# Kernel tuning notes

Measured on AMD Instinct MI355X. Metric: run time of the kernel, lower is better.

Reference implementation:

```python
import jax, jax.numpy as jnp
import numpy as np

N = 200_000      # active voxels
C_IN = 128
C_OUT = 128
GRID = 128
K = 27           # 3x3x3 submanifold kernel offsets
EPS = 1e-4       # scn BatchNormalization default eps
LEAK = 0.333     # scn LeakyReLU default leakiness


def _build_neighbor_idx(rng):
    # unique active voxel coords via unique linear keys in GRID^3
    keys = rng.choice(GRID ** 3, size=N, replace=False).astype(np.int64)
    z = keys % GRID
    y = (keys // GRID) % GRID
    x = keys // (GRID * GRID)
    coords = np.stack([x, y, z], axis=1)  # [N,3]
    order = np.argsort(keys)
    sorted_keys = keys[order]
    offs = np.array([(dx, dy, dz) for dx in (-1, 0, 1)
                     for dy in (-1, 0, 1) for dz in (-1, 0, 1)], dtype=np.int64)
    nb = np.full((N, K), -1, dtype=np.int32)
    for k in range(K):
        q = coords + offs[k]  # [N,3]
        inb = np.all((q >= 0) & (q < GRID), axis=1)
        qk = (q[:, 0] * GRID + q[:, 1]) * GRID + q[:, 2]
        pos = np.searchsorted(sorted_keys, qk)
        pos = np.clip(pos, 0, N - 1)
        hit = inb & (sorted_keys[pos] == qk)
        nb[:, k] = np.where(hit, order[pos].astype(np.int32), -1)
    return nb


def setup_inputs() -> dict:
    key = jax.random.key(0)
    k1, k2 = jax.random.split(key)
    rng = np.random.default_rng(0)
    neighbor_idx = jnp.asarray(_build_neighbor_idx(rng))       # [N,27] int32, -1 = inactive
    features = jax.random.normal(k1, (N, C_IN), dtype=jnp.float32)
    # per-offset conv weights, scn-style init scale
    W = jax.random.normal(k2, (K, C_IN, C_OUT), dtype=jnp.float32) * (1.0 / np.sqrt(K * C_IN))
    b = jnp.zeros((C_OUT,), dtype=jnp.float32)
    gamma = jnp.ones((C_OUT,), dtype=jnp.float32)
    beta = jnp.zeros((C_OUT,), dtype=jnp.float32)
    return {"features": features, "W": W, "b": b, "gamma": gamma,
            "beta": beta, "neighbor_idx": neighbor_idx}


def reference(features, W, b, gamma, beta, neighbor_idx):
    # Submanifold 3D conv: output only at active sites; gather active neighbors.
    valid = (neighbor_idx >= 0)                      # [N,27] bool
    idx = jnp.where(valid, neighbor_idx, 0)          # safe gather index
    out = jnp.broadcast_to(b, (features.shape[0], C_OUT))
    for k in range(K):  # fixed structural loop over 27 kernel offsets
        xk = features[idx[:, k]] * valid[:, k:k + 1].astype(features.dtype)  # [N,C_IN]
        out = out + xk @ W[k]                                                # [N,C_OUT]
    # BatchNormalization over all active sites (training-mode batch stats)
    mean = jnp.mean(out, axis=0)
    var = jnp.var(out, axis=0)
    out = (out - mean) * jax.lax.rsqrt(var + EPS) * gamma + beta
    # LeakyReLU (scn default leakiness 0.333)
    return jnp.where(out > 0, out, LEAK * out)
```

## Files before the change

kernel.cpp:

```cpp
#include <hip/hip_runtime.h>
#include <hip/hip_bf16.h>

#define N_VOX 200000
#define CI 128
#define CO 128
#define KK 27
#define BM 128
#define NBLK 1563
#define NSTEP 54
#define LEAK 0.333f
#define BN_EPS 1e-4f

typedef unsigned short u16;
typedef unsigned int u32;
typedef __attribute__((ext_vector_type(8))) short short8;
typedef __attribute__((ext_vector_type(4))) float f32x4;

typedef const __attribute__((address_space(1))) u32* gptr_t;
typedef __attribute__((address_space(3))) u32* lptr_t;

__device__ __forceinline__ u16 f2bf(float f) {
  union { float f; u32 u; } x; x.f = f;
  return (u16)((x.u + 0x7FFFu + ((x.u >> 16) & 1u)) >> 16);
}
__device__ __forceinline__ u16 cvt_bf(float f) {
  union { __hip_bfloat16 h; u16 u; } c;
  c.h = __float2bfloat16(f);
  return c.u;
}

__global__ __launch_bounds__(256) void fcast_kernel(const float* __restrict__ f,
                                                    u16* __restrict__ fb) {
  size_t i = ((size_t)blockIdx.x * 256 + threadIdx.x) * 8;
  float4 a = *(const float4*)(f + i);
  float4 b = *(const float4*)(f + i + 4);
  u16 t[8];
  t[0] = cvt_bf(a.x); t[1] = cvt_bf(a.y); t[2] = cvt_bf(a.z); t[3] = cvt_bf(a.w);
  t[4] = cvt_bf(b.x); t[5] = cvt_bf(b.y); t[6] = cvt_bf(b.z); t[7] = cvt_bf(b.w);
  *(uint4*)(fb + i) = *(const uint4*)t;
}

__global__ __launch_bounds__(256) void wcast2_kernel(const float* __restrict__ W,
                                                     u16* __restrict__ Wt2) {
  int gid = blockIdx.x * 256 + threadIdx.x;
  int lane = gid & 63, chunk = gid >> 6;
  int n8 = chunk & 7, ks = (chunk >> 3) & 1, half = (chunk >> 4) & 1, k = chunk >> 5;
  int lr = lane & 15, lg = lane >> 4;
  int co = n8 * 16 + lr;
  int ci0 = half * 64 + ks * 32 + lg * 8;
  const float* Wk = W + (size_t)k * CI * CO;
  u16 t[8];
#pragma unroll
  for (int e = 0; e < 8; ++e) t[e] = f2bf(Wk[(ci0 + e) * CO + co]);
  *(uint4*)(Wt2 + (size_t)gid * 8) = *(const uint4*)t;
}

__global__ __launch_bounds__(256, 2) void conv_kernel(
    const u16* __restrict__ featb, const u16* __restrict__ Wt2,
    const int* __restrict__ nb, const u16* __restrict__ zp,
    float* __restrict__ out, float* __restrict__ partial) {
  __shared__ __align__(16) char smem[79360];
  int* const nbs = (int*)(smem + 65536);
  float* const sq = (float*)smem;

  const int tid = threadIdx.x;
  const int bid = blockIdx.x;
  const int row0 = bid * BM;

  for (int i = tid; i < BM * KK; i += 256) {
    int gi = row0 * KK + i;
    nbs[i] = (gi < N_VOX * KK) ? nb[gi] : -1;
  }
  __syncthreads();

  const int lane = tid & 63;
  const int wv = tid >> 6;
  const int wr = wv >> 1, wc = wv & 1;
  const int lr = lane & 15, lg = lane >> 4;

  f32x4 acc[4][4];
#pragma unroll
  for (int m = 0; m < 4; ++m)
#pragma unroll
    for (int n = 0; n < 4; ++n) acc[m][n] = (f32x4){0.f, 0.f, 0.f, 0.f};

  short8 b0[8], b1[8];

  auto issueA = [&](int s, int slot) {
    if (s >= NSTEP) s = NSTEP - 1;
    int k = s >> 1;
    int halfU = (s & 1) * 64;
    u16* Adst = (u16*)(smem + slot * 16384);
    int r = tid >> 3, cl = tid & 7;
#pragma unroll
    for (int j = 0; j < 4; ++j) {
      int row = j * 32 + r;
      int src = nbs[row * KK + k];
      const u16* g = (src >= 0) ? (featb + (size_t)src * CI + halfU) : zp;
      g += ((cl ^ (row & 7)) << 3);
      __builtin_amdgcn_global_load_lds((gptr_t)g, (lptr_t)(Adst + (j * 32 + wv * 8) * 64),
                                       16, 0, 0);
    }
  };

  auto loadB = [&](int s, short8* bn) {
    if (s >= NSTEP) s = NSTEP - 1;
    int k = s >> 1, half = s & 1;
    const u16* base = Wt2 + (((k * 2 + half) * 16 + wc * 4) * 512) + lane * 8;
#pragma unroll
    for (int n = 0; n < 4; ++n)
#pragma unroll
      for (int ks = 0; ks < 2; ++ks)
        bn[n * 2 + ks] = *(const short8*)(base + (ks * 8 + n) * 512);
  };

  auto compute = [&](int slot, const short8* bc) {
    const char* A = smem + slot * 16384;
    __builtin_amdgcn_s_setprio(1);
#pragma unroll
    for (int ks = 0; ks < 2; ++ks) {
      short8 a[4];
#pragma unroll
      for (int m = 0; m < 4; ++m) {
        int r = wr * 64 + m * 16 + lr;
        a[m] = *(const short8*)(A + r * 128 + ((ks * 64 + lg * 16) ^ ((r & 7) << 4)));
      }
#pragma unroll
      for (int m = 0; m < 4; ++m)
#pragma unroll
        for (int n = 0; n < 4; ++n)
          acc[m][n] = __builtin_amdgcn_mfma_f32_16x16x32_bf16(a[m], bc[n * 2 + ks],
                                                              acc[m][n], 0, 0, 0);
    }
    __builtin_amdgcn_s_setprio(0);
  };

  auto step_body = [&](int s, const short8* bc, short8* bn) {
    asm volatile("s_waitcnt vmcnt(16)" ::: "memory");
    __builtin_amdgcn_sched_barrier(0);
    __builtin_amdgcn_s_barrier();
    __builtin_amdgcn_sched_barrier(0);
    loadB(s + 1, bn);
    issueA(s + 3, (s + 3) & 3);
    compute(s & 3, bc);
  };

  issueA(0, 0);
  issueA(1, 1);
  loadB(0, b0);
  issueA(2, 2);
  for (int s = 0; s < NSTEP; s += 2) {
    step_body(s, b0, b1);
    step_body(s + 1, b1, b0);
  }

  float sv[4], qv[4];
#pragma unroll
  for (int n = 0; n < 4; ++n) {
    float s = 0.f, q = 0.f;
    int col = wc * 64 + n * 16 + lr;
#pragma unroll
    for (int m = 0; m < 4; ++m) {
      int rb = row0 + wr * 64 + m * 16 + lg * 4;
#pragma unroll
      for (int e = 0; e < 4; ++e) {
        float x = acc[m][n][e];
        if (rb + e < N_VOX) out[(size_t)(rb + e) * CO + col] = x;
        s += x; q += x * x;
      }
    }
    s += __shfl_xor(s, 16, 64); s += __shfl_xor(s, 32, 64);
    q += __shfl_xor(q, 16, 64); q += __shfl_xor(q, 32, 64);
    sv[n] = s; qv[n] = q;
  }
  __syncthreads();
  if (lg == 0) {
#pragma unroll
    for (int n = 0; n < 4; ++n) {
      int col = wc * 64 + n * 16 + lr;
      sq[wr * 256 + col] = sv[n];
      sq[wr * 256 + 128 + col] = qv[n];
    }
  }
  __syncthreads();
  partial[(size_t)bid * 256 + tid] = sq[tid] + sq[256 + tid];
}

__global__ __launch_bounds__(256, 2) void conv_fb_kernel(
    const float* __restrict__ feat, const u16* __restrict__ Wt2,
    const int* __restrict__ nb, float* __restrict__ out,
    float* __restrict__ partial) {
  __shared__ __align__(16) char smem[46592];
  u16* const Ab = (u16*)smem;
  int* const nbs = (int*)(smem + 32768);
  float* const sq = (float*)smem;

  const int tid = threadIdx.x;
  const int bid = blockIdx.x;
  const int row0 = bid * BM;

  for (int i = tid; i < BM * KK; i += 256) {
    int gi = row0 * KK + i;
    nbs[i] = (gi < N_VOX * KK) ? nb[gi] : -1;
  }
  __syncthreads();

  const int lane = tid & 63;
  const int wv = tid >> 6;
  const int wr = wv >> 1, wc = wv & 1;
  const int lr = lane & 15, lg = lane >> 4;
  const int arow = tid >> 1;
  const int acol = (tid & 1) * 32;

  f32x4 acc[4][4];
#pragma unroll
  for (int m = 0; m < 4; ++m)
#pragma unroll
    for (int n = 0; n < 4; ++n) acc[m][n] = (f32x4){0.f, 0.f, 0.f, 0.f};

  float4 af[8];
  short8 b0[8], b1[8];

  auto issueAf = [&](int s) {
    int k = s >> 1, half = (s & 1) * 64;
    int src = nbs[arow * KK + k];
    if (src >= 0) {
      const float4* p = (const float4*)(feat + (size_t)src * CI + half + acol);
#pragma unroll
      for (int j = 0; j < 8; ++j) af[j] = p[j];
    } else {
#pragma unroll
      for (int j = 0; j < 8; ++j) af[j] = (float4){0.f, 0.f, 0.f, 0.f};
    }
  };
  auto loadB = [&](int s, short8* bn) {
    int k = s >> 1, half = s & 1;
    const u16* base = Wt2 + (((k * 2 + half) * 16 + wc * 4) * 512) + lane * 8;
#pragma unroll
    for (int n = 0; n < 4; ++n)
#pragma unroll
      for (int ks = 0; ks < 2; ++ks)
        bn[n * 2 + ks] = *(const short8*)(base + (ks * 8 + n) * 512);
  };
  auto writeA = [&](u16* Adst) {
    int v = arow & 7;
#pragma unroll
    for (int q = 0; q < 4; ++q) {
      u16 t8[8];
#pragma unroll
      for (int i = 0; i < 2; ++i) {
        float4 f = af[q * 2 + i];
        t8[i * 4 + 0] = cvt_bf(f.x); t8[i * 4 + 1] = cvt_bf(f.y);
        t8[i * 4 + 2] = cvt_bf(f.z); t8[i * 4 + 3] = cvt_bf(f.w);
      }
      int c_o = (tid & 1) * 4 + q;
      *(uint4*)&Adst[arow * 64 + ((c_o ^ v) << 3)] = *(const uint4*)t8;
    }
  };
  auto compute = [&](const u16* A, const short8* bc) {
#pragma unroll
    for (int ks = 0; ks < 2; ++ks) {
      short8 a[4];
#pragma unroll
      for (int m = 0; m < 4; ++m) {
        int r = wr * 64 + m * 16 + lr;
        a[m] = *(const short8*)((const char*)A + r * 128 +
                                ((ks * 64 + lg * 16) ^ ((r & 7) << 4)));
      }
#pragma unroll
      for (int m = 0; m < 4; ++m)
#pragma unroll
        for (int n = 0; n < 4; ++n)
          acc[m][n] = __builtin_amdgcn_mfma_f32_16x16x32_bf16(a[m], bc[n * 2 + ks],
                                                              acc[m][n], 0, 0, 0);
    }
  };

  issueAf(0);
  loadB(0, b0);
  for (int s = 0; s + 2 <= NSTEP - 1; s += 2) {
    writeA(Ab + (s & 1) * 8192); __syncthreads();
    issueAf(s + 1); loadB(s + 1, b1);
    compute(Ab + (s & 1) * 8192, b0);
    writeA(Ab + ((s + 1) & 1) * 8192); __syncthreads();
    issueAf(s + 2); loadB(s + 2, b0);
    compute(Ab + ((s + 1) & 1) * 8192, b1);
  }
  writeA(Ab); __syncthreads();
  issueAf(NSTEP - 1); loadB(NSTEP - 1, b1);
  compute(Ab, b0);
  writeA(Ab + 8192); __syncthreads();
  compute(Ab + 8192, b1);

  float sv[4], qv[4];
#pragma unroll
  for (int n = 0; n < 4; ++n) {
    float s = 0.f, q = 0.f;
    int col = wc * 64 + n * 16 + lr;
#pragma unroll
    for (int m = 0; m < 4; ++m) {
      int rb = row0 + wr * 64 + m * 16 + lg * 4;
#pragma unroll
      for (int e = 0; e < 4; ++e) {
        float x = acc[m][n][e];
        if (rb + e < N_VOX) out[(size_t)(rb + e) * CO + col] = x;
        s += x; q += x * x;
      }
    }
    s += __shfl_xor(s, 16, 64); s += __shfl_xor(s, 32, 64);
    q += __shfl_xor(q, 16, 64); q += __shfl_xor(q, 32, 64);
    sv[n] = s; qv[n] = q;
  }
  __syncthreads();
  if (lg == 0) {
#pragma unroll
    for (int n = 0; n < 4; ++n) {
      int col = wc * 64 + n * 16 + lr;
      sq[wr * 256 + col] = sv[n];
      sq[wr * 256 + 128 + col] = qv[n];
    }
  }
  __syncthreads();
  partial[(size_t)bid * 256 + tid] = sq[tid] + sq[256 + tid];
}

__global__ __launch_bounds__(256) void reduce1_kernel(const float* __restrict__ partial,
                                                      float* __restrict__ partial2) {
  int t = threadIdx.x, b = blockIdx.x;
  float acc = 0.f;
  int jend = (b + 1) * 16; if (jend > NBLK) jend = NBLK;
  for (int j = b * 16; j < jend; ++j) acc += partial[(size_t)j * 256 + t];
  partial2[(size_t)b * 256 + t] = acc;
}

__global__ __launch_bounds__(256) void reduce2_kernel(const float* __restrict__ partial2,
                                                      const float* __restrict__ gamma,
                                                      const float* __restrict__ beta,
                                                      float* __restrict__ stats) {
  __shared__ float sums[256];
  int t = threadIdx.x;
  float acc = 0.f;
  for (int j = 0; j < 98; ++j) acc += partial2[(size_t)j * 256 + t];
  sums[t] = acc;
  __syncthreads();
  if (t < 128) {
    float mean = sums[t] / (float)N_VOX;
    float var = sums[128 + t] / (float)N_VOX - mean * mean;
    float scale = gamma[t] * rsqrtf(var + BN_EPS);
    stats[t] = scale;
    stats[128 + t] = beta[t] - mean * scale;
  }
}

__global__ __launch_bounds__(256) void bnact_kernel(float* __restrict__ out,
                                                    const float* __restrict__ stats) {
  __shared__ float s_scale[128], s_shift[128];
  int t = threadIdx.x;
  if (t < 128) { s_scale[t] = stats[t]; s_shift[t] = stats[128 + t]; }
  __syncthreads();
  size_t i = (size_t)blockIdx.x * 256 + t;
  float4* o4 = (float4*)out;
  float4 v = o4[i];
  int c0 = ((int)(i & 31)) << 2;
  float x;
  x = v.x * s_scale[c0 + 0] + s_shift[c0 + 0]; v.x = x > 0.f ? x : LEAK * x;
  x = v.y * s_scale[c0 + 1] + s_shift[c0 + 1]; v.y = x > 0.f ? x : LEAK * x;
  x = v.z * s_scale[c0 + 2] + s_shift[c0 + 2]; v.z = x > 0.f ? x : LEAK * x;
  x = v.w * s_scale[c0 + 3] + s_shift[c0 + 3]; v.w = x > 0.f ? x : LEAK * x;
  o4[i] = v;
}

extern "C" void kernel_launch(void* const* d_in, const int* in_sizes, int n_in,
                              void* d_out, int out_size, void* d_ws, size_t ws_size,
                              hipStream_t stream) {
  const float* feat  = (const float*)d_in[0];
  const float* W     = (const float*)d_in[1];
  const float* gamma = (const float*)d_in[3];
  const float* beta  = (const float*)d_in[4];
  const int*   nb    = (const int*)d_in[5];
  float* out = (float*)d_out;

  char* ws = (char*)d_ws;
  u16*   Wt2      = (u16*)ws;
  float* partial  = (float*)(ws + 884736);
  float* partial2 = (float*)(ws + 2485248);
  float* stats    = (float*)(ws + 2585600);
  u16*   zp       = (u16*)(ws + 2586624);
  u16*   featb    = (u16*)(ws + 2586880);
  const size_t need_fast = 2586880u + 51200000u;

  hipLaunchKernelGGL(wcast2_kernel, dim3(216), dim3(256), 0, stream, W, Wt2);
  if (ws_size >= need_fast) {
    hipMemsetAsync(zp, 0, 256, stream);
    hipLaunchKernelGGL(fcast_kernel, dim3(12500), dim3(256), 0, stream, feat, featb);
    hipLaunchKernelGGL(conv_kernel, dim3(NBLK), dim3(256), 0, stream,
                       featb, Wt2, nb, zp, out, partial);
  } else {
    hipLaunchKernelGGL(conv_fb_kernel, dim3(NBLK), dim3(256), 0, stream,
                       feat, Wt2, nb, out, partial);
  }
  hipLaunchKernelGGL(reduce1_kernel, dim3(98), dim3(256), 0, stream, partial, partial2);
  hipLaunchKernelGGL(reduce2_kernel, dim3(1), dim3(256), 0, stream, partial2, gamma, beta, stats);
  hipLaunchKernelGGL(bnact_kernel, dim3(25000), dim3(256), 0, stream, out, stats);
}
```

Measured before the change: 303.7 us.

## Compact valid neighbors per offset and skip inactive rows in sparse conv

The dense conv kernel, which gathered all 128 rows for every one of the 27 offsets, is replaced by a sparse variant. Per block it uses ballots to compact the valid (row, source) pairs for each offset into LDS lists padded to multiples of 16. It then runs MFMA only over those compacted tiles and scatter-accumulates the results into an LDS fp32 accumulator, with the centre offset handled first as a plain store. Weights are re-laid out so each wave keeps its own 32-column slice in registers per offset. The aim is to cut MFMA and gather work in proportion to neighbor sparsity. In exchange it drops the async LDS pipelining and caps each offset list at 64 entries, which would silently drop neighbors in denser inputs.

Measured after the change: 294.5 us. 3.0% less time.

```diff
diff --git a/kernel.cpp b/kernel.cpp
--- a/kernel.cpp
+++ b/kernel.cpp
@@ -10,6 +10,8 @@
 #define NSTEP 54
 #define LEAK 0.333f
 #define BN_EPS 1e-4f
+#define SENT 0x3FFFFu
+#define ACC_STRIDE 132
 
 typedef unsigned short u16;
 typedef unsigned int u32;
@@ -40,154 +42,151 @@
   *(uint4*)(fb + i) = *(const uint4*)t;
 }
 
-__global__ __launch_bounds__(256) void wcast2_kernel(const float* __restrict__ W,
-                                                     u16* __restrict__ Wt2) {
+__global__ __launch_bounds__(256) void wcast3_kernel(const float* __restrict__ W,
+                                                     u16* __restrict__ Wt3) {
   int gid = blockIdx.x * 256 + threadIdx.x;
   int lane = gid & 63, chunk = gid >> 6;
-  int n8 = chunk & 7, ks = (chunk >> 3) & 1, half = (chunk >> 4) & 1, k = chunk >> 5;
+  int ks = chunk & 3, nf = (chunk >> 2) & 7, k = chunk >> 5;
   int lr = lane & 15, lg = lane >> 4;
-  int co = n8 * 16 + lr;
-  int ci0 = half * 64 + ks * 32 + lg * 8;
+  int co = nf * 16 + lr;
+  int ci0 = ks * 32 + lg * 8;
   const float* Wk = W + (size_t)k * CI * CO;
   u16 t[8];
 #pragma unroll
   for (int e = 0; e < 8; ++e) t[e] = f2bf(Wk[(ci0 + e) * CO + co]);
-  *(uint4*)(Wt2 + (size_t)gid * 8) = *(const uint4*)t;
-}
-
-__global__ __launch_bounds__(256, 2) void conv_kernel(
-    const u16* __restrict__ featb, const u16* __restrict__ Wt2,
+  *(uint4*)(Wt3 + (size_t)gid * 8) = *(const uint4*)t;
+}
+
+__global__ __launch_bounds__(256, 2) void conv_sp_kernel(
+    const u16* __restrict__ featb, const u16* __restrict__ Wt3,
     const int* __restrict__ nb, const u16* __restrict__ zp,
     float* __restrict__ out, float* __restrict__ partial) {
-  __shared__ __align__(16) char smem[79360];
-  int* const nbs = (int*)(smem + 65536);
-  float* const sq = (float*)smem;
+  __shared__ __align__(16) char smem[75776];
+  float* const accf = (float*)smem;
+  u32* const rb_lds = (u32*)(smem + 67584);
+  int* const cnt_lds = (int*)(smem + 74752);
+  int* const wcnt = (int*)(smem + 74864);
+  float* const ps = (float*)(smem + 67584);
 
   const int tid = threadIdx.x;
   const int bid = blockIdx.x;
   const int row0 = bid * BM;
-
-  for (int i = tid; i < BM * KK; i += 256) {
-    int gi = row0 * KK + i;
-    nbs[i] = (gi < N_VOX * KK) ? nb[gi] : -1;
-  }
-  __syncthreads();
-
   const int lane = tid & 63;
-  const int wv = tid >> 6;
-  const int wr = wv >> 1, wc = wv & 1;
+  const int w = tid >> 6;
+
+  {
+    const bool inrow = (tid < 128) && (row0 + tid < N_VOX);
+    const int* nbp = nb + (size_t)(row0 + tid) * KK;
+    int vv[KK];
+#pragma unroll
+    for (int k = 0; k < KK; ++k) vv[k] = (k != 13 && inrow) ? nbp[k] : -1;
+    if (tid < 128)
+      rb_lds[832 + tid] = ((u32)tid << 18) | (inrow ? (u32)(row0 + tid) : SENT);
+    if (tid == 0) cnt_lds[13] = 128;
+#pragma unroll
+    for (int k = 0; k < KK; ++k) {
+      if (k == 13) continue;
+      bool valid = vv[k] >= 0;
+      unsigned long long m = __ballot(valid);
+      if (lane == 0) wcnt[w] = (int)__popcll(m);
+      __syncthreads();
+      int pos = (int)__popcll(m & ((1ull << lane) - 1ull)) + (w == 1 ? wcnt[0] : 0);
+      int cnt = wcnt[0] + wcnt[1]; if (cnt > 64) cnt = 64;
+      int kbase = (k < 13) ? k * 64 : 960 + (k - 14) * 64;
+      if (valid && pos < 64) rb_lds[kbase + pos] = ((u32)tid << 18) | (u32)vv[k];
+      int pe = (cnt + 15) & ~15;
+      for (int i = cnt + tid; i < pe; i += 256) rb_lds[kbase + i] = SENT;
+      if (tid == 0) cnt_lds[k] = cnt;
+      __syncthreads();
+    }
+  }
+
+  const int wv = w;
   const int lr = lane & 15, lg = lane >> 4;
-
-  f32x4 acc[4][4];
-#pragma unroll
-  for (int m = 0; m < 4; ++m)
-#pragma unroll
-    for (int n = 0; n < 4; ++n) acc[m][n] = (f32x4){0.f, 0.f, 0.f, 0.f};
-
-  short8 b0[8], b1[8];
-
-  auto issueA = [&](int s, int slot) {
-    if (s >= NSTEP) s = NSTEP - 1;
-    int k = s >> 1;
-    int halfU = (s & 1) * 64;
-    u16* Adst = (u16*)(smem + slot * 16384);
-    int r = tid >> 3, cl = tid & 7;
-#pragma unroll
-    for (int j = 0; j < 4; ++j) {
-      int row = j * 32 + r;
-      int src = nbs[row * KK + k];
-      const u16* g = (src >= 0) ? (featb + (size_t)src * CI + halfU) : zp;
-      g += ((cl ^ (row & 7)) << 3);
-      __builtin_amdgcn_global_load_lds((gptr_t)g, (lptr_t)(Adst + (j * 32 + wv * 8) * 64),
-                                       16, 0, 0);
-    }
-  };
-
-  auto loadB = [&](int s, short8* bn) {
-    if (s >= NSTEP) s = NSTEP - 1;
-    int k = s >> 1, half = s & 1;
-    const u16* base = Wt2 + (((k * 2 + half) * 16 + wc * 4) * 512) + lane * 8;
-#pragma unroll
-    for (int n = 0; n < 4; ++n)
-#pragma unroll
-      for (int ks = 0; ks < 2; ++ks)
-        bn[n * 2 + ks] = *(const short8*)(base + (ks * 8 + n) * 512);
-  };
-
-  auto compute = [&](int slot, const short8* bc) {
-    const char* A = smem + slot * 16384;
-    __builtin_amdgcn_s_setprio(1);
-#pragma unroll
-    for (int ks = 0; ks < 2; ++ks) {
+  const int colbase = wv * 32 + lr;
+
+  for (int kk = 0; kk < KK; ++kk) {
+    const int k = (kk == 0) ? 13 : (kk <= 13 ? kk - 1 : kk);
+    const int kbase = (k < 13) ? k * 64 : (k == 13 ? 832 : 960 + (k - 14) * 64);
+    const int cnt = cnt_lds[k];
+    if (cnt == 0) continue;
+    const int nt = (cnt + 15) >> 4;
+    short8 b0[4], b1[4];
+    {
+      const u16* wb = Wt3 + (size_t)(k * 32 + wv * 8) * 512 + lane * 8;
+#pragma unroll
+      for (int ks = 0; ks < 4; ++ks) {
+        b0[ks] = *(const short8*)(wb + ks * 512);
+        b1[ks] = *(const short8*)(wb + (4 + ks) * 512);
+      }
+    }
+    for (int t = 0; t < nt; ++t) {
+      u32 es = rb_lds[kbase + t * 16 + lr];
+      u32 src = es & SENT;
+      const u16* ap = (src == SENT) ? zp : (featb + (size_t)src * CI);
       short8 a[4];
 #pragma unroll
-      for (int m = 0; m < 4; ++m) {
-        int r = wr * 64 + m * 16 + lr;
-        a[m] = *(const short8*)(A + r * 128 + ((ks * 64 + lg * 16) ^ ((r & 7) << 4)));
-      }
-#pragma unroll
-      for (int m = 0; m < 4; ++m)
-#pragma unroll
-        for (int n = 0; n < 4; ++n)
-          acc[m][n] = __builtin_amdgcn_mfma_f32_16x16x32_bf16(a[m], bc[n * 2 + ks],
-                                                              acc[m][n], 0, 0, 0);
-    }
-    __builtin_amdgcn_s_setprio(0);
-  };
-
-  auto step_body = [&](int s, const short8* bc, short8* bn) {
-    asm volatile("s_waitcnt vmcnt(16)" ::: "memory");
-    __builtin_amdgcn_sched_barrier(0);
-    __builtin_amdgcn_s_barrier();
-    __builtin_amdgcn_sched_barrier(0);
-    loadB(s + 1, bn);
-    issueA(s + 3, (s + 3) & 3);
-    compute(s & 3, bc);
-  };
-
-  issueA(0, 0);
-  issueA(1, 1);
-  loadB(0, b0);
-  issueA(2, 2);
-  for (int s = 0; s < NSTEP; s += 2) {
-    step_body(s, b0, b1);
-    step_body(s + 1, b1, b0);
-  }
-
-  float sv[4], qv[4];
-#pragma unroll
-  for (int n = 0; n < 4; ++n) {
-    float s = 0.f, q = 0.f;
-    int col = wc * 64 + n * 16 + lr;
-#pragma unroll
-    for (int m = 0; m < 4; ++m) {
-      int rb = row0 + wr * 64 + m * 16 + lg * 4;
-#pragma unroll
-      for (int e = 0; e < 4; ++e) {
-        float x = acc[m][n][e];
-        if (rb + e < N_VOX) out[(size_t)(rb + e) * CO + col] = x;
-        s += x; q += x * x;
-      }
-    }
-    s += __shfl_xor(s, 16, 64); s += __shfl_xor(s, 32, 64);
-    q += __shfl_xor(q, 16, 64); q += __shfl_xor(q, 32, 64);
-    sv[n] = s; qv[n] = q;
-  }
-  __syncthreads();
-  if (lg == 0) {
-#pragma unroll
-    for (int n = 0; n < 4; ++n) {
-      int col = wc * 64 + n * 16 + lr;
-      sq[wr * 256 + col] = sv[n];
-      sq[wr * 256 + 128 + col] = qv[n];
-    }
-  }
-  __syncthreads();
-  partial[(size_t)bid * 256 + tid] = sq[tid] + sq[256 + tid];
+      for (int ks = 0; ks < 4; ++ks) a[ks] = *(const short8*)(ap + ks * 32 + lg * 8);
+      f32x4 c0 = {0.f, 0.f, 0.f, 0.f}, c1 = {0.f, 0.f, 0.f, 0.f};
+#pragma unroll
+      for (int ks = 0; ks < 4; ++ks) {
+        c0 = __builtin_amdgcn_mfma_f32_16x16x32_bf16(a[ks], b0[ks], c0, 0, 0, 0);
+        c1 = __builtin_amdgcn_mfma_f32_16x16x32_bf16(a[ks], b1[ks], c1, 0, 0, 0);
+      }
+      if (kk == 0) {
+#pragma unroll
+        for (int r = 0; r < 4; ++r) {
+          int dr = (int)(rb_lds[kbase + t * 16 + lg * 4 + r] >> 18);
+          accf[dr * ACC_STRIDE + colbase] = c0[r];
+          accf[dr * ACC_STRIDE + colbase + 16] = c1[r];
+        }
+      } else {
+#pragma unroll
+        for (int r = 0; r < 4; ++r) {
+          u32 e2 = rb_lds[kbase + t * 16 + lg * 4 + r];
+          if (e2 != SENT) {
+            int dr = (int)(e2 >> 18);
+            accf[dr * ACC_STRIDE + colbase] += c0[r];
+            accf[dr * ACC_STRIDE + colbase + 16] += c1[r];
+          }
+        }
+      }
+    }
+  }
+  __syncthreads();
+
+  float s4[4] = {0.f, 0.f, 0.f, 0.f}, q4[4] = {0.f, 0.f, 0.f, 0.f};
+  const int col4 = (tid & 31) * 4;
+  const int rgrp = tid >> 5;
+#pragma unroll
+  for (int i = 0; i < 16; ++i) {
+    int row = rgrp + i * 8;
+    f32x4 v = *(const f32x4*)&accf[row * ACC_STRIDE + col4];
+    int grow = row0 + row;
+    if (grow < N_VOX) {
+      *(float4*)&out[(size_t)grow * CO + col4] = *(float4*)&v;
+#pragma unroll
+      for (int j = 0; j < 4; ++j) { s4[j] += v[j]; q4[j] += v[j] * v[j]; }
+    }
+  }
+  __syncthreads();
+#pragma unroll
+  for (int j = 0; j < 4; ++j) {
+    ps[rgrp * 128 + col4 + j] = s4[j];
+    ps[1024 + rgrp * 128 + col4 + j] = q4[j];
+  }
+  __syncthreads();
+  {
+    int col = tid & 127, which = tid >> 7;
+    float acc = 0.f;
+#pragma unroll
+    for (int g = 0; g < 8; ++g) acc += ps[which * 1024 + g * 128 + col];
+    partial[(size_t)bid * 256 + tid] = acc;
+  }
 }
 
 __global__ __launch_bounds__(256, 2) void conv_fb_kernel(
-    const float* __restrict__ feat, const u16* __restrict__ Wt2,
+    const float* __restrict__ feat, const u16* __restrict__ Wt3,
     const int* __restrict__ nb, float* __restrict__ out,
     float* __restrict__ partial) {
   __shared__ __align__(16) char smem[46592];
@@ -235,12 +234,12 @@
   };
   auto loadB = [&](int s, short8* bn) {
     int k = s >> 1, half = s & 1;
-    const u16* base = Wt2 + (((k * 2 + half) * 16 + wc * 4) * 512) + lane * 8;
 #pragma unroll
     for (int n = 0; n < 4; ++n)
 #pragma unroll
       for (int ks = 0; ks < 2; ++ks)
-        bn[n * 2 + ks] = *(const short8*)(base + (ks * 8 + n) * 512);
+        bn[n * 2 + ks] = *(const short8*)(Wt3 +
+            (size_t)((k * 32 + (wc * 4 + n) * 4) + half * 2 + ks) * 512 + lane * 8);
   };
   auto writeA = [&](u16* Adst) {
     int v = arow & 7;
@@ -299,11 +298,11 @@
     int col = wc * 64 + n * 16 + lr;
 #pragma unroll
     for (int m = 0; m < 4; ++m) {
-      int rb = row0 + wr * 64 + m * 16 + lg * 4;
+      int rb_ = row0 + wr * 64 + m * 16 + lg * 4;
 #pragma unroll
       for (int e = 0; e < 4; ++e) {
         float x = acc[m][n][e];
-        if (rb + e < N_VOX) out[(size_t)(rb + e) * CO + col] = x;
+        if (rb_ + e < N_VOX) out[(size_t)(rb_ + e) * CO + col] = x;
         s += x; q += x * x;
       }
     }
@@ -381,23 +380,23 @@
   float* out = (float*)d_out;
 
   char* ws = (char*)d_ws;
-  u16*   Wt2      = (u16*)ws;
+  u16*   Wt3      = (u16*)ws;
   float* partial  = (float*)(ws + 884736);
   float* partial2 = (float*)(ws + 2485248);
   float* stats    = (float*)(ws + 2585600);
   u16*   zp       = (u16*)(ws + 2586624);
   u16*   featb    = (u16*)(ws + 2586880);
-  const size_t need_fast = 2586880u + 51200000u;
-
-  hipLaunchKernelGGL(wcast2_kernel, dim3(216), dim3(256), 0, stream, W, Wt2);
+  const size_t need_fast = 53786880u;
+
+  hipLaunchKernelGGL(wcast3_kernel, dim3(216), dim3(256), 0, stream, W, Wt3);
   if (ws_size >= need_fast) {
     hipMemsetAsync(zp, 0, 256, stream);
     hipLaunchKernelGGL(fcast_kernel, dim3(12500), dim3(256), 0, stream, feat, featb);
-    hipLaunchKernelGGL(conv_kernel, dim3(NBLK), dim3(256), 0, stream,
-                       featb, Wt2, nb, zp, out, partial);
+    hipLaunchKernelGGL(conv_sp_kernel, dim3(NBLK), dim3(256), 0, stream,
+                       featb, Wt3, nb, zp, out, partial);
   } else {
     hipLaunchKernelGGL(conv_fb_kernel, dim3(NBLK), dim3(256), 0, stream,
-                       feat, Wt2, nb, out, partial);
+                       feat, Wt3, nb, out, partial);
   }
   hipLaunchKernelGGL(reduce1_kernel, dim3(98), dim3(256), 0, stream, partial, partial2);
   hipLaunchKernelGGL(reduce2_kernel, dim3(1), dim3(256), 0, stream, partial2, gamma, beta, stats);
```

## Stage weights through LDS with 512-thread blocks and triple-buffered A/B pipeline

Applied to the files above, without the earlier changes.

The main conv kernel now uses 512-thread blocks with 8 waves, each wave computing a 32x64 sub-tile. Weight tiles are staged into LDS with global_load_lds alongside the gathered feature rows, in a 3-slot ring buffer, instead of being loaded into registers per wave. A new transposed, XOR-swizzled weight cast kernel supports this layout, and block IDs are remapped so each XCD gets a contiguous range of rows, which should improve L2 locality of neighbor gathers. The change cuts register pressure and duplicated B loads across waves. In exchange it adds an extra barrier per half-step and uses far more LDS per block, which may limit occupancy.

Result: slower. 360.0 us (+18.5%).

```diff
diff --git a/kernel.cpp b/kernel.cpp
--- a/kernel.cpp
+++ b/kernel.cpp
@@ -40,119 +40,137 @@
   *(uint4*)(fb + i) = *(const uint4*)t;
 }
 
-__global__ __launch_bounds__(256) void wcast2_kernel(const float* __restrict__ W,
-                                                     u16* __restrict__ Wt2) {
+__global__ __launch_bounds__(256) void wcast_kernel(const float* __restrict__ W,
+                                                    u16* __restrict__ Wt) {
+  __shared__ float tile[32][33];
+  int k = blockIdx.z;
+  int ci0 = blockIdx.y * 32, co0 = blockIdx.x * 32;
+  const float* Wk = W + (size_t)k * CI * CO;
+  u16* Wtk = Wt + (size_t)k * CI * CO;
+  int tx = threadIdx.x, ty = threadIdx.y;
+#pragma unroll
+  for (int j = 0; j < 4; ++j)
+    tile[ty + j * 8][tx] = Wk[(ci0 + ty + j * 8) * CO + co0 + tx];
+  __syncthreads();
+#pragma unroll
+  for (int j = 0; j < 4; ++j) {
+    int co = co0 + ty + j * 8;
+    int ci = ci0 + tx;
+    Wtk[co * CI + (ci ^ ((co & 7) << 3))] = f2bf(tile[tx][ty + j * 8]);
+  }
+}
+
+__global__ __launch_bounds__(256) void wcast3_kernel(const float* __restrict__ W,
+                                                     u16* __restrict__ Wt3) {
   int gid = blockIdx.x * 256 + threadIdx.x;
   int lane = gid & 63, chunk = gid >> 6;
-  int n8 = chunk & 7, ks = (chunk >> 3) & 1, half = (chunk >> 4) & 1, k = chunk >> 5;
+  int ks = chunk & 3, nf = (chunk >> 2) & 7, k = chunk >> 5;
   int lr = lane & 15, lg = lane >> 4;
-  int co = n8 * 16 + lr;
-  int ci0 = half * 64 + ks * 32 + lg * 8;
+  int co = nf * 16 + lr;
+  int ci0 = ks * 32 + lg * 8;
   const float* Wk = W + (size_t)k * CI * CO;
   u16 t[8];
 #pragma unroll
   for (int e = 0; e < 8; ++e) t[e] = f2bf(Wk[(ci0 + e) * CO + co]);
-  *(uint4*)(Wt2 + (size_t)gid * 8) = *(const uint4*)t;
-}
-
-__global__ __launch_bounds__(256, 2) void conv_kernel(
-    const u16* __restrict__ featb, const u16* __restrict__ Wt2,
+  *(uint4*)(Wt3 + (size_t)gid * 8) = *(const uint4*)t;
+}
+
+__global__ __launch_bounds__(512, 2) void conv_dn_kernel(
+    const u16* __restrict__ featb, const u16* __restrict__ Wt,
     const int* __restrict__ nb, const u16* __restrict__ zp,
     float* __restrict__ out, float* __restrict__ partial) {
-  __shared__ __align__(16) char smem[79360];
-  int* const nbs = (int*)(smem + 65536);
-  float* const sq = (float*)smem;
+  __shared__ __align__(16) char smem[112128];
+  int* const nbs = (int*)(smem + 98304);
+  float* const ps = (float*)smem;
 
   const int tid = threadIdx.x;
-  const int bid = blockIdx.x;
+  const int orig = blockIdx.x;
+  const int xcd = orig & 7, oidx = orig >> 3;
+  const int bid = (xcd < 3) ? xcd * 196 + oidx : 588 + (xcd - 3) * 195 + oidx;
   const int row0 = bid * BM;
-
-  for (int i = tid; i < BM * KK; i += 256) {
+  const int lane = tid & 63;
+  const int w = tid >> 6;
+  const int wr = w >> 1, wc = w & 1;
+  const int lr = lane & 15, lg = lane >> 4;
+
+  for (int i = tid; i < BM * KK; i += 512) {
     int gi = row0 * KK + i;
     nbs[i] = (gi < N_VOX * KK) ? nb[gi] : -1;
   }
   __syncthreads();
 
-  const int lane = tid & 63;
-  const int wv = tid >> 6;
-  const int wr = wv >> 1, wc = wv & 1;
-  const int lr = lane & 15, lg = lane >> 4;
-
-  f32x4 acc[4][4];
-#pragma unroll
-  for (int m = 0; m < 4; ++m)
+  f32x4 acc[2][4];
+#pragma unroll
+  for (int m = 0; m < 2; ++m)
 #pragma unroll
     for (int n = 0; n < 4; ++n) acc[m][n] = (f32x4){0.f, 0.f, 0.f, 0.f};
 
-  short8 b0[8], b1[8];
-
-  auto issueA = [&](int s, int slot) {
-    if (s >= NSTEP) s = NSTEP - 1;
-    int k = s >> 1;
-    int halfU = (s & 1) * 64;
-    u16* Adst = (u16*)(smem + slot * 16384);
-    int r = tid >> 3, cl = tid & 7;
-#pragma unroll
-    for (int j = 0; j < 4; ++j) {
-      int row = j * 32 + r;
+  auto stage = [&](int s, int slot) {
+    int k = s >> 1, half = (s & 1) * 64;
+    u16* Aslot = (u16*)(smem + slot * 32768);
+    u16* Bslot = Aslot + 8192;
+#pragma unroll
+    for (int j = 0; j < 2; ++j) {
+      int cid = j * 512 + tid;
+      int row = cid >> 3, c = cid & 7;
       int src = nbs[row * KK + k];
-      const u16* g = (src >= 0) ? (featb + (size_t)src * CI + halfU) : zp;
-      g += ((cl ^ (row & 7)) << 3);
-      __builtin_amdgcn_global_load_lds((gptr_t)g, (lptr_t)(Adst + (j * 32 + wv * 8) * 64),
-                                       16, 0, 0);
-    }
-  };
-
-  auto loadB = [&](int s, short8* bn) {
-    if (s >= NSTEP) s = NSTEP - 1;
-    int k = s >> 1, half = s & 1;
-    const u16* base = Wt2 + (((k * 2 + half) * 16 + wc * 4) * 512) + lane * 8;
-#pragma unroll
-    for (int n = 0; n < 4; ++n)
-#pragma unroll
-      for (int ks = 0; ks < 2; ++ks)
-        bn[n * 2 + ks] = *(const short8*)(base + (ks * 8 + n) * 512);
-  };
-
-  auto compute = [&](int slot, const short8* bc) {
-    const char* A = smem + slot * 16384;
+      const u16* g = (src >= 0) ? (featb + (size_t)src * CI + half) : zp;
+      g += ((c ^ (row & 7)) << 3);
+      __builtin_amdgcn_global_load_lds((gptr_t)g,
+          (lptr_t)(Aslot + (j * 512 + w * 64) * 8), 16, 0, 0);
+    }
+#pragma unroll
+    for (int j = 0; j < 2; ++j) {
+      int cid = j * 512 + tid;
+      int co = cid >> 3, sub = cid & 7;
+      __builtin_amdgcn_global_load_lds(
+          (gptr_t)(Wt + (size_t)k * CI * CO + co * CI + half + sub * 8),
+          (lptr_t)(Bslot + (j * 512 + w * 64) * 8), 16, 0, 0);
+    }
+  };
+
+  auto phase = [&](const u16* A, const u16* B, int ks) {
+    short8 a[2], b[4];
+#pragma unroll
+    for (int m = 0; m < 2; ++m) {
+      int r = wr * 32 + m * 16 + lr;
+      a[m] = *(const short8*)((const char*)(A + r * 64) +
+                              ((ks * 64 + lg * 16) ^ ((r & 7) << 4)));
+    }
+#pragma unroll
+    for (int n = 0; n < 4; ++n) {
+      int cn = wc * 64 + n * 16 + lr;
+      b[n] = *(const short8*)((const char*)(B + cn * 64) +
+                              ((ks * 64 + lg * 16) ^ ((cn & 7) << 4)));
+    }
     __builtin_amdgcn_s_setprio(1);
 #pragma unroll
-    for (int ks = 0; ks < 2; ++ks) {
-      short8 a[4];
-#pragma unroll
-      for (int m = 0; m < 4; ++m) {
-        int r = wr * 64 + m * 16 + lr;
-        a[m] = *(const short8*)(A + r * 128 + ((ks * 64 + lg * 16) ^ ((r & 7) << 4)));
-      }
-#pragma unroll
-      for (int m = 0; m < 4; ++m)
-#pragma unroll
-        for (int n = 0; n < 4; ++n)
-          acc[m][n] = __builtin_amdgcn_mfma_f32_16x16x32_bf16(a[m], bc[n * 2 + ks],
-                                                              acc[m][n], 0, 0, 0);
-    }
+    for (int m = 0; m < 2; ++m)
+#pragma unroll
+      for (int n = 0; n < 4; ++n)
+        acc[m][n] = __builtin_amdgcn_mfma_f32_16x16x32_bf16(a[m], b[n], acc[m][n], 0, 0, 0);
     __builtin_amdgcn_s_setprio(0);
   };
 
-  auto step_body = [&](int s, const short8* bc, short8* bn) {
-    asm volatile("s_waitcnt vmcnt(16)" ::: "memory");
+  stage(0, 0);
+  stage(1, 1);
+  for (int s = 0; s < NSTEP; ++s) {
+    asm volatile("s_waitcnt vmcnt(4)" ::: "memory");
     __builtin_amdgcn_sched_barrier(0);
     __builtin_amdgcn_s_barrier();
     __builtin_amdgcn_sched_barrier(0);
-    loadB(s + 1, bn);
-    issueA(s + 3, (s + 3) & 3);
-    compute(s & 3, bc);
-  };
-
-  issueA(0, 0);
-  issueA(1, 1);
-  loadB(0, b0);
-  issueA(2, 2);
-  for (int s = 0; s < NSTEP; s += 2) {
-    step_body(s, b0, b1);
-    step_body(s + 1, b1, b0);
-  }
+    int sn = (s + 2 < NSTEP) ? s + 2 : NSTEP - 1;
+    stage(sn, (s + 2) % 3);
+    const u16* A = (const u16*)(smem + (s % 3) * 32768);
+    const u16* B = A + 8192;
+    phase(A, B, 0);
+    __builtin_amdgcn_sched_barrier(0);
+    __builtin_amdgcn_s_barrier();
+    __builtin_amdgcn_sched_barrier(0);
+    phase(A, B, 1);
+  }
+  asm volatile("s_waitcnt vmcnt(0)" ::: "memory");
+  __syncthreads();
 
   float sv[4], qv[4];
 #pragma unroll
@@ -160,13 +178,15 @@
     float s = 0.f, q = 0.f;
     int col = wc * 64 + n * 16 + lr;
 #pragma unroll
-    for (int m = 0; m < 4; ++m) {
-      int rb = row0 + wr * 64 + m * 16 + lg * 4;
+    for (int m = 0; m < 2; ++m) {
+      int rb = row0 + wr * 32 + m * 16 + lg * 4;
 #pragma unroll
       for (int e = 0; e < 4; ++e) {
         float x = acc[m][n][e];
-        if (rb + e < N_VOX) out[(size_t)(rb + e) * CO + col] = x;
-        s += x; q += x * x;
+        if (rb + e < N_VOX) {
+          out[(size_t)(rb + e) * CO + col] = x;
+          s += x; q += x * x;
+        }
       }
     }
     s += __shfl_xor(s, 16, 64); s += __shfl_xor(s, 32, 64);
@@ -178,16 +198,21 @@
 #pragma unroll
     for (int n = 0; n < 4; ++n) {
       int col = wc * 64 + n * 16 + lr;
-      sq[wr * 256 + col] = sv[n];
-      sq[wr * 256 + 128 + col] = qv[n];
-    }
-  }
-  __syncthreads();
-  partial[(size_t)bid * 256 + tid] = sq[tid] + sq[256 + tid];
+      ps[wr * 256 + col] = sv[n];
+      ps[wr * 256 + 128 + col] = qv[n];
+    }
+  }
+  __syncthreads();
+  if (tid < 256) {
+    float acc2 = 0.f;
+#pragma unroll
+    for (int g = 0; g < 4; ++g) acc2 += ps[g * 256 + tid];
+    partial[(size_t)bid * 256 + tid] = acc2;
+  }
 }
 
 __global__ __launch_bounds__(256, 2) void conv_fb_kernel(
-    const float* __restrict__ feat, const u16* __restrict__ Wt2,
+    const float* __restrict__ feat, const u16* __restrict__ Wt3,
     const int* __restrict__ nb, float* __restrict__ out,
     float* __restrict__ partial) {
   __shared__ __align__(16) char smem[46592];
@@ -197,9 +222,9 @@
 
   const int tid = threadIdx.x;
   const int bid = blockIdx.x;
-  const int row0 = bid * BM;
-
-  for (int i = tid; i < BM * KK; i += 256) {
+  const int row0 = bid * 128;
+
+  for (int i = tid; i < 128 * KK; i += 256) {
     int gi = row0 * KK + i;
     nbs[i] = (gi < N_VOX * KK) ? nb[gi] : -1;
   }
@@ -235,12 +260,12 @@
   };
   auto loadB = [&](int s, short8* bn) {
     int k = s >> 1, half = s & 1;
-    const u16* base = Wt2 + (((k * 2 + half) * 16 + wc * 4) * 512) + lane * 8;
 #pragma unroll
     for (int n = 0; n < 4; ++n)
 #pragma unroll
       for (int ks = 0; ks < 2; ++ks)
-        bn[n * 2 + ks] = *(const short8*)(base + (ks * 8 + n) * 512);
+        bn[n * 2 + ks] = *(const short8*)(Wt3 +
+            (size_t)((k * 32 + (wc * 4 + n) * 4) + half * 2 + ks) * 512 + lane * 8);
   };
   auto writeA = [&](u16* Adst) {
     int v = arow & 7;
@@ -299,11 +324,11 @@
     int col = wc * 64 + n * 16 + lr;
 #pragma unroll
     for (int m = 0; m < 4; ++m) {
-      int rb = row0 + wr * 64 + m * 16 + lg * 4;
+      int rb_ = row0 + wr * 64 + m * 16 + lg * 4;
 #pragma unroll
       for (int e = 0; e < 4; ++e) {
         float x = acc[m][n][e];
-        if (rb + e < N_VOX) out[(size_t)(rb + e) * CO + col] = x;
+        if (rb_ + e < N_VOX) out[(size_t)(rb_ + e) * CO + col] = x;
         s += x; q += x * x;
       }
     }
@@ -325,10 +350,11 @@
 }
 
 __global__ __launch_bounds__(256) void reduce1_kernel(const float* __restrict__ partial,
-                                                      float* __restrict__ partial2) {
+                                                      float* __restrict__ partial2,
+                                                      int nblk) {
   int t = threadIdx.x, b = blockIdx.x;
   float acc = 0.f;
-  int jend = (b + 1) * 16; if (jend > NBLK) jend = NBLK;
+  int jend = (b + 1) * 16; if (jend > nblk) jend = nblk;
   for (int j = b * 16; j < jend; ++j) acc += partial[(size_t)j * 256 + t];
   partial2[(size_t)b * 256 + t] = acc;
 }
@@ -336,11 +362,11 @@
 __global__ __launch_bounds__(256) void reduce2_kernel(const float* __restrict__ partial2,
                                                       const float* __restrict__ gamma,
                                                       const float* __restrict__ beta,
-                                                      float* __restrict__ stats) {
+                                                      float* __restrict__ stats, int n2) {
   __shared__ float sums[256];
   int t = threadIdx.x;
   float acc = 0.f;
-  for (int j = 0; j < 98; ++j) acc += partial2[(size_t)j * 256 + t];
+  for (int j = 0; j < n2; ++j) acc += partial2[(size_t)j * 256 + t];
   sums[t] = acc;
   __syncthreads();
   if (t < 128) {
@@ -381,25 +407,32 @@
   float* out = (float*)d_out;
 
   char* ws = (char*)d_ws;
-  u16*   Wt2      = (u16*)ws;
+  u16*   Wt       = (u16*)ws;
   float* partial  = (float*)(ws + 884736);
   float* partial2 = (float*)(ws + 2485248);
   float* stats    = (float*)(ws + 2585600);
   u16*   zp       = (u16*)(ws + 2586624);
   u16*   featb    = (u16*)(ws + 2586880);
-  const size_t need_fast = 2586880u + 51200000u;
-
-  hipLaunchKernelGGL(wcast2_kernel, dim3(216), dim3(256), 0, stream, W, Wt2);
+  const size_t need_fast = 53786880u;
+
   if (ws_size >= need_fast) {
+    hipLaunchKernelGGL(wcast_kernel, dim3(4, 4, 27), dim3(32, 8), 0, stream, W, Wt);
     hipMemsetAsync(zp, 0, 256, stream);
     hipLaunchKernelGGL(fcast_kernel, dim3(12500), dim3(256), 0, stream, feat, featb);
-    hipLaunchKernelGGL(conv_kernel, dim3(NBLK), dim3(256), 0, stream,
-                       featb, Wt2, nb, zp, out, partial);
+    hipLaunchKernelGGL(conv_dn_kernel, dim3(NBLK), dim3(512), 0, stream,
+                       featb, Wt, nb, zp, out, partial);
+    hipLaunchKernelGGL(reduce1_kernel, dim3(98), dim3(256), 0, stream,
+                       partial, partial2, NBLK);
+    hipLaunchKernelGGL(reduce2_kernel, dim3(1), dim3(256), 0, stream,
+                       partial2, gamma, beta, stats, 98);
   } else {
+    hipLaunchKernelGGL(wcast3_kernel, dim3(216), dim3(256), 0, stream, W, Wt);
     hipLaunchKernelGGL(conv_fb_kernel, dim3(NBLK), dim3(256), 0, stream,
-                       feat, Wt2, nb, out, partial);
-  }
-  hipLaunchKernelGGL(reduce1_kernel, dim3(98), dim3(256), 0, stream, partial, partial2);
-  hipLaunchKernelGGL(reduce2_kernel, dim3(1), dim3(256), 0, stream, partial2, gamma, beta, stats);
+                       feat, Wt, nb, out, partial);
+    hipLaunchKernelGGL(reduce1_kernel, dim3(98), dim3(256), 0, stream,
+                       partial, partial2, NBLK);
+    hipLaunchKernelGGL(reduce2_kernel, dim3(1), dim3(256), 0, stream,
+                       partial2, gamma, beta, stats, 98);
+  }
   hipLaunchKernelGGL(bnact_kernel, dim3(25000), dim3(256), 0, stream, out, stats);
 }
```
